# Performance work log

Hardware: AMD Instinct MI355X
Metric: run time of the kernel (lower is better)

Reference implementation:

```python
import jax, jax.numpy as jnp
import numpy as np

B, S, H, NH = 2, 2048, 4096, 32
HD = H // NH  # head_dim = 128
ROPE_BASE = 10000.0


def setup_inputs() -> dict:
    key = jax.random.key(0)
    k1, k2, k3 = jax.random.split(key, 3)
    hidden_states = jax.random.normal(k1, (B, S, H), dtype=jnp.float32)
    w_qkv = jax.random.normal(k2, (H, 3 * H), dtype=jnp.float32) * 0.02
    w_o = jax.random.normal(k3, (H, H), dtype=jnp.float32) * 0.02
    position_ids = jnp.broadcast_to(jnp.arange(S, dtype=jnp.int32), (B, S))
    return {"hidden_states": hidden_states, "w_qkv": w_qkv, "w_o": w_o,
            "position_ids": position_ids}


def _rope_neox(x, cos, sin):
    # x: [B,S,NH,HD]; cos/sin: [B,S,1,HD//2]. NeoX rotate-halves.
    half = HD // 2
    x1, x2 = x[..., :half], x[..., half:]
    return jnp.concatenate([x1 * cos - x2 * sin, x2 * cos + x1 * sin], axis=-1)


def reference(hidden_states, w_qkv, w_o, position_ids):
    # fused QKV projection (stands in for quantized WQLinear)
    qkv = hidden_states @ w_qkv                        # [B,S,3H]
    q, k, v = jnp.split(qkv, 3, axis=-1)
    q = q.reshape(B, S, NH, HD)
    k = k.reshape(B, S, NH, HD)
    v = v.reshape(B, S, NH, HD)

    # NeoX rotary embedding indexed by position_ids
    inv_freq = 1.0 / (ROPE_BASE ** (jnp.arange(0, HD, 2, dtype=jnp.float32) / HD))
    freqs = position_ids.astype(jnp.float32)[..., None] * inv_freq  # [B,S,HD/2]
    cos = jnp.cos(freqs)[:, :, None, :]
    sin = jnp.sin(freqs)[:, :, None, :]
    q = _rope_neox(q, cos, sin)
    k = _rope_neox(k, cos, sin)

    # causal SDPA (prefill path: past_key_value is None -> is_causal=True)
    scale = 1.0 / jnp.sqrt(jnp.asarray(HD, dtype=q.dtype))
    scores = jnp.einsum('bqhd,bkhd->bhqk', q, k) * scale  # [B,NH,S,S]
    causal = jnp.tril(jnp.ones((S, S), dtype=bool))
    scores = jnp.where(causal, scores, jnp.finfo(scores.dtype).min)
    probs = jax.nn.softmax(scores, axis=-1)
    attn = jnp.einsum('bhqk,bkhd->bqhd', probs, v).reshape(B, S, H)

    return attn @ w_o  # [B,S,H]
```

## Files before the change

kernel.cpp:

```cpp
#include <hip/hip_runtime.h>
#include <stdint.h>
#include <math.h>

#define B_ 2
#define S_ 2048
#define H_ 4096
#define NH_ 32
#define HD_ 128

using s16x8 = __attribute__((ext_vector_type(8))) short;
using f32x4 = __attribute__((ext_vector_type(4))) float;

__device__ __forceinline__ unsigned short f2b(float f) {
  union { float f; unsigned u; } v; v.f = f;
  unsigned r = v.u + 0x7FFFu + ((v.u >> 16) & 1u);
  return (unsigned short)(r >> 16);
}
__device__ __forceinline__ unsigned short f2b_trunc(float f) {
  union { float f; unsigned u; } v; v.f = f;
  return (unsigned short)(v.u >> 16);
}
__device__ __forceinline__ float b2f(unsigned short h) {
  union { unsigned u; float f; } v; v.u = ((unsigned)h) << 16;
  return v.f;
}

__device__ __forceinline__ void async_cp16(const void* g, void* l) {
  __builtin_amdgcn_global_load_lds(
      (__attribute__((address_space(1))) void*)(void*)g,
      (__attribute__((address_space(3))) void*)l, 16, 0, 0);
}

#define MFMA16(a, b, c) __builtin_amdgcn_mfma_f32_16x16x32_bf16((a), (b), (c), 0, 0, 0)
#define BARRIER() asm volatile("s_barrier" ::: "memory")

__global__ void cast_f32_bf16(const float* __restrict__ in,
                              unsigned short* __restrict__ out, long n) {
  long i = ((long)blockIdx.x * 256 + threadIdx.x) * 4;
  if (i >= n) return;
  const float4 v = *(const float4*)(in + i);
  ushort4 o;
  o.x = f2b(v.x); o.y = f2b(v.y); o.z = f2b(v.z); o.w = f2b(v.w);
  *(ushort4*)(out + i) = o;
}

__global__ void transpose_cast_4096(const float* __restrict__ in,
                                    unsigned short* __restrict__ out, int in_stride) {
  __shared__ unsigned tile[64][33];
  const int t = threadIdx.x;
  const int c0 = blockIdx.x * 64;
  const int r0 = blockIdx.y * 64;
  const int l16 = t & 15, q = t >> 4;
  const int c4 = l16 * 4;
#pragma unroll
  for (int ii = 0; ii < 2; ii++) {
    const int p = q + ii * 16;
    const float4 ra = *(const float4*)&in[(long)(r0 + 2 * p) * in_stride + c0 + c4];
    const float4 rb = *(const float4*)&in[(long)(r0 + 2 * p + 1) * in_stride + c0 + c4];
    tile[c4 + 0][p] = (unsigned)f2b(ra.x) | ((unsigned)f2b(rb.x) << 16);
    tile[c4 + 1][p] = (unsigned)f2b(ra.y) | ((unsigned)f2b(rb.y) << 16);
    tile[c4 + 2][p] = (unsigned)f2b(ra.z) | ((unsigned)f2b(rb.z) << 16);
    tile[c4 + 3][p] = (unsigned)f2b(ra.w) | ((unsigned)f2b(rb.w) << 16);
  }
  __syncthreads();
  const int c = t >> 2, r8 = (t & 3) * 8;
  unsigned v[8];
#pragma unroll
  for (int k = 0; k < 8; k++) v[k] = tile[c][r8 + k];
  uint4 o0 = {v[0], v[1], v[2], v[3]};
  uint4 o1 = {v[4], v[5], v[6], v[7]};
  unsigned short* dst = &out[(long)(c0 + c) * 4096 + r0 + 2 * r8];
  *(uint4*)dst = o0;
  *(uint4*)(dst + 8) = o1;
}

template <int MODE>
__global__ __launch_bounds__(512, 2) void gemm_bt(
    const unsigned short* __restrict__ A,
    const unsigned short* __restrict__ Bt,
    float* __restrict__ Cf,
    unsigned short* __restrict__ Dst,
    int M, int N, int K) {
  __shared__ __align__(16) unsigned short lds[65536];
  const int tid = threadIdx.x;
  const int lane = tid & 63;
  const int w = tid >> 6;
  const int quad = lane >> 4, l16 = lane & 15;
  const int wm = w >> 2, wn = w & 3;

  const int id = blockIdx.x;
  const int swz = (id & 7) * 32 + (id >> 3);
  const int m0 = (swz >> 4) * 256;
  const int n0 = (swz & 15) * 256;

  const int lr = tid >> 3;
  const int c8 = (tid & 7) * 8;
  const int csw = c8 ^ (((lr >> 1) & 7) << 3);
  const unsigned short* gA = A + (long)(m0 + lr) * K + csw;
  const unsigned short* gB = Bt + (long)(n0 + lr) * K + csw;
  const long K64 = (long)K * 64;
  const int ldsS = lr * 64 + c8;

  const int fsw = ((l16 >> 1) & 7) << 3;
  const int colk0 = (quad * 8) ^ fsw;
  const int colk1 = colk0 ^ 32;
  const int aoff0 = (wm * 128 + l16) * 64 + colk0;
  const int aoff1 = (wm * 128 + l16) * 64 + colk1;
  const int boff0 = 32768 + (wn * 64 + l16) * 64 + colk0;
  const int boff1 = 32768 + (wn * 64 + l16) * 64 + colk1;

  const f32x4 z4 = {0.f, 0.f, 0.f, 0.f};
  f32x4 acc[8][4];
#pragma unroll
  for (int mi = 0; mi < 8; mi++)
#pragma unroll
    for (int ni = 0; ni < 4; ni++) acc[mi][ni] = z4;

  async_cp16(gB, &lds[32768 + ldsS]);
  async_cp16(gB + K64, &lds[32768 + ldsS + 4096]);
  async_cp16(gB + 2 * K64, &lds[32768 + 8192 + ldsS]);
  async_cp16(gB + 3 * K64, &lds[32768 + 8192 + ldsS + 4096]);
  async_cp16(gA, &lds[ldsS]);
  async_cp16(gA + K64, &lds[ldsS + 4096]);
  async_cp16(gA + 2 * K64, &lds[8192 + ldsS]);
  async_cp16(gA + 3 * K64, &lds[8192 + ldsS + 4096]);
  async_cp16(gB + 64, &lds[32768 + 16384 + ldsS]);
  async_cp16(gB + 64 + K64, &lds[32768 + 16384 + ldsS + 4096]);
  async_cp16(gB + 64 + 2 * K64, &lds[32768 + 16384 + 8192 + ldsS]);
  async_cp16(gB + 64 + 3 * K64, &lds[32768 + 16384 + 8192 + ldsS + 4096]);
  asm volatile("s_waitcnt vmcnt(4)\n\ts_barrier" ::: "memory");

  const int NT = 64;
  for (int t = 0; t < NT; ++t) {
    const int buf = (t & 1) * 16384;
    const int nbuf = 16384 - buf;
    const long kA = (long)(t + 1) * 64;
    const long kB = (long)(t + 2) * 64;
    s16x8 a[4][2], b0[2][2], b1[2][2];

#pragma unroll
    for (int mi = 0; mi < 4; ++mi) {
      a[mi][0] = *(const s16x8*)&lds[buf + aoff0 + mi * 1024];
      a[mi][1] = *(const s16x8*)&lds[buf + aoff1 + mi * 1024];
    }
#pragma unroll
    for (int ni = 0; ni < 2; ++ni) {
      b0[ni][0] = *(const s16x8*)&lds[buf + boff0 + ni * 1024];
      b0[ni][1] = *(const s16x8*)&lds[buf + boff1 + ni * 1024];
    }
    if (t < NT - 1) {
      async_cp16(gA + kA, &lds[nbuf + ldsS]);
      async_cp16(gA + kA + K64, &lds[nbuf + ldsS + 4096]);
    }
    BARRIER();
    __builtin_amdgcn_s_setprio(1);
#pragma unroll
    for (int mi = 0; mi < 4; ++mi)
#pragma unroll
      for (int ni = 0; ni < 2; ++ni) {
        acc[mi][ni] = MFMA16(a[mi][0], b0[ni][0], acc[mi][ni]);
        acc[mi][ni] = MFMA16(a[mi][1], b0[ni][1], acc[mi][ni]);
      }
    __builtin_amdgcn_s_setprio(0);
    BARRIER();

#pragma unroll
    for (int ni = 0; ni < 2; ++ni) {
      b1[ni][0] = *(const s16x8*)&lds[buf + boff0 + (ni + 2) * 1024];
      b1[ni][1] = *(const s16x8*)&lds[buf + boff1 + (ni + 2) * 1024];
    }
    if (t < NT - 1) {
      async_cp16(gA + kA + 2 * K64, &lds[nbuf + 8192 + ldsS]);
      async_cp16(gA + kA + 3 * K64, &lds[nbuf + 8192 + ldsS + 4096]);
    }
    BARRIER();
    __builtin_amdgcn_s_setprio(1);
#pragma unroll
    for (int mi = 0; mi < 4; ++mi)
#pragma unroll
      for (int ni = 0; ni < 2; ++ni) {
        acc[mi][ni + 2] = MFMA16(a[mi][0], b1[ni][0], acc[mi][ni + 2]);
        acc[mi][ni + 2] = MFMA16(a[mi][1], b1[ni][1], acc[mi][ni + 2]);
      }
    __builtin_amdgcn_s_setprio(0);
    BARRIER();

#pragma unroll
    for (int mi = 0; mi < 4; ++mi) {
      a[mi][0] = *(const s16x8*)&lds[buf + aoff0 + (mi + 4) * 1024];
      a[mi][1] = *(const s16x8*)&lds[buf + aoff1 + (mi + 4) * 1024];
    }
    if (t < NT - 2) {
      async_cp16(gB + kB, &lds[32768 + buf + ldsS]);
      async_cp16(gB + kB + K64, &lds[32768 + buf + ldsS + 4096]);
    }
    BARRIER();
    __builtin_amdgcn_s_setprio(1);
#pragma unroll
    for (int mi = 0; mi < 4; ++mi)
#pragma unroll
      for (int ni = 0; ni < 2; ++ni) {
        acc[mi + 4][ni + 2] = MFMA16(a[mi][0], b1[ni][0], acc[mi + 4][ni + 2]);
        acc[mi + 4][ni + 2] = MFMA16(a[mi][1], b1[ni][1], acc[mi + 4][ni + 2]);
      }
    __builtin_amdgcn_s_setprio(0);
    BARRIER();

    if (t < NT - 2) {
      async_cp16(gB + kB + 2 * K64, &lds[32768 + buf + 8192 + ldsS]);
      async_cp16(gB + kB + 3 * K64, &lds[32768 + buf + 8192 + ldsS + 4096]);
    }
    BARRIER();
    __builtin_amdgcn_s_setprio(1);
#pragma unroll
    for (int mi = 0; mi < 4; ++mi)
#pragma unroll
      for (int ni = 0; ni < 2; ++ni) {
        acc[mi + 4][ni] = MFMA16(a[mi][0], b0[ni][0], acc[mi + 4][ni]);
        acc[mi + 4][ni] = MFMA16(a[mi][1], b0[ni][1], acc[mi + 4][ni]);
      }
    __builtin_amdgcn_s_setprio(0);
    if (t < NT - 2) {
      asm volatile("s_waitcnt vmcnt(4)\n\ts_barrier" ::: "memory");
    } else if (t == NT - 2) {
      asm volatile("s_waitcnt vmcnt(0)\n\ts_barrier" ::: "memory");
    } else {
      BARRIER();
    }
  }

#pragma unroll
  for (int mi = 0; mi < 8; ++mi)
#pragma unroll
    for (int ni = 0; ni < 4; ++ni) {
      const int row = m0 + wm * 128 + mi * 16 + quad * 4;
      const int col = n0 + wn * 64 + ni * 16 + l16;
      if (MODE == 0) {
#pragma unroll
        for (int r = 0; r < 4; ++r)
          Cf[(long)(row + r) * N + col] = acc[mi][ni][r];
      } else {
        const int h = col >> 7, d = col & 127;
#pragma unroll
        for (int r = 0; r < 4; ++r) {
          const int m = row + r;
          const int b = m >> 11, s = m & 2047;
          Dst[((long)((b * NH_ + h) * S_) + s) * HD_ + d] = f2b(acc[mi][ni][r]);
        }
      }
    }
}

__global__ void rope_kernel(unsigned short* __restrict__ Qb,
                            unsigned short* __restrict__ Kb,
                            const int* __restrict__ pos_ids) {
  const float QSCALE = 1.4426950408889634f * 0.08838834764831845f;
  const long idx = (long)blockIdx.x * 256 + threadIdx.x;
  const int i = (int)(idx & 63);
  const long row = idx >> 6;
  const int s = (int)(row & (S_ - 1));
  const long bh = row >> 11;
  const int b = (int)(bh >> 5);
  const float pos = (float)pos_ids[b * S_ + s];
  const float inv = exp2f(-(float)i * 0.20762050593046f);
  const float ang = pos * inv;
  const float sn = sinf(ang), cs = cosf(ang);
  const long base = row * HD_;
  const float q1 = b2f(Qb[base + i]), q2 = b2f(Qb[base + 64 + i]);
  Qb[base + i] = f2b((q1 * cs - q2 * sn) * QSCALE);
  Qb[base + 64 + i] = f2b((q2 * cs + q1 * sn) * QSCALE);
  const float k1 = b2f(Kb[base + i]), k2 = b2f(Kb[base + 64 + i]);
  Kb[base + i] = f2b(k1 * cs - k2 * sn);
  Kb[base + 64 + i] = f2b(k2 * cs + k1 * sn);
}

__global__ void transpose_v(const unsigned short* __restrict__ V,
                            unsigned short* __restrict__ Vt) {
  __shared__ unsigned short tile[64][66];
  const int bh = blockIdx.z;
  const int s0 = blockIdx.x * 64;
  const int d0 = blockIdx.y * 64;
  const unsigned short* src = V + (long)bh * S_ * HD_;
  unsigned short* dst = Vt + (long)bh * S_ * HD_;
  const int tx = threadIdx.x & 63, ty = threadIdx.x >> 6;
#pragma unroll
  for (int i = 0; i < 64; i += 4)
    tile[ty + i][tx] = src[(long)(s0 + ty + i) * HD_ + d0 + tx];
  __syncthreads();
#pragma unroll
  for (int i = 0; i < 64; i += 4)
    dst[(long)(d0 + ty + i) * S_ + s0 + tx] = tile[tx][ty + i];
}

__global__ __launch_bounds__(256, 2) void flash_attn(
    const unsigned short* __restrict__ Qb,
    const unsigned short* __restrict__ Kb,
    const unsigned short* __restrict__ Vt,
    unsigned short* __restrict__ Ab) {
  __shared__ __align__(16) unsigned short Ks[16 * 64 * 8];
  __shared__ __align__(16) unsigned short Vs[8 * 128 * 8];
  __shared__ __align__(16) unsigned short plds[128 * 72];
  const int tid = threadIdx.x;
  const int w = tid >> 6, lane = tid & 63;
  const int quad = lane >> 4, l16 = lane & 15;
  const int qx = blockIdx.y;
  const int bh = blockIdx.x;
  const int b = bh >> 5, h = bh & 31;

  const unsigned short* Qh = Qb + (long)bh * S_ * HD_;
  const unsigned short* Kh = Kb + (long)bh * S_ * HD_;
  const unsigned short* Vh = Vt + (long)bh * S_ * HD_;

  const unsigned short* kstage = Kh + (long)(tid & 63) * HD_ + (tid >> 6) * 8;
  const unsigned short* vstage = Vh + (long)(tid & 127) * S_ + (tid >> 7) * 8;

  const f32x4 z4 = {0.f, 0.f, 0.f, 0.f};
  s16x8 onesv;
#pragma unroll
  for (int j = 0; j < 8; j++) onesv[j] = (short)0x3F80;

  for (int half = 0; half < 2; half++) {
    const int qt = half ? qx : 15 - qx;
    const int q0 = qt * 128;
    const int wq = q0 + w * 32;

    s16x8 qf[2][4];
#pragma unroll
    for (int rb = 0; rb < 2; rb++)
#pragma unroll
      for (int ks = 0; ks < 4; ks++)
        qf[rb][ks] = *(const s16x8*)(Qh + (long)(wq + rb * 16 + l16) * HD_ + ks * 32 + quad * 8);

    f32x4 oacc[2][8];
    f32x4 lacc[2];
#pragma unroll
    for (int rb = 0; rb < 2; rb++) {
#pragma unroll
      for (int oc = 0; oc < 8; oc++) oacc[rb][oc] = z4;
      lacc[rb] = z4;
    }
    float mrow[2][4];
#pragma unroll
    for (int rb = 0; rb < 2; rb++)
#pragma unroll
      for (int r = 0; r < 4; r++) mrow[rb][r] = -3.0e38f;

    const int nkt = 2 * qt + 2;

    for (int kt = 0; kt < nkt; kt++) {
      const int kbase = kt * 64;
      __syncthreads();
#pragma unroll
      for (int j = 0; j < 4; j++)
        async_cp16(kstage + (long)kbase * HD_ + j * 32, &Ks[(j * 256 + tid) * 8]);
#pragma unroll
      for (int j = 0; j < 4; j++)
        async_cp16(vstage + kbase + j * 16, &Vs[(j * 256 + tid) * 8]);
      __syncthreads();

      const bool active = (kbase < wq + 32);
      if (active) {
        f32x4 sacc[2][4];
#pragma unroll
        for (int rb = 0; rb < 2; rb++)
#pragma unroll
          for (int ni = 0; ni < 4; ni++) sacc[rb][ni] = z4;
        __builtin_amdgcn_s_setprio(1);
#pragma unroll
        for (int ni = 0; ni < 4; ni++) {
#pragma unroll
          for (int ks = 0; ks < 4; ks++) {
            const s16x8 kf = *(const s16x8*)&Ks[((ks * 4 + quad) * 64 + ni * 16 + l16) * 8];
            sacc[0][ni] = MFMA16(qf[0][ks], kf, sacc[0][ni]);
            sacc[1][ni] = MFMA16(qf[1][ks], kf, sacc[1][ni]);
          }
        }
        __builtin_amdgcn_s_setprio(0);

        const bool band = (kbase + 64 > wq);
        float pm[2][4];
        bool small_ = true;
#pragma unroll
        for (int rb = 0; rb < 2; rb++) {
          const int rloc = w * 32 + rb * 16 + quad * 4;
          if (band) {
#pragma unroll
            for (int ni = 0; ni < 4; ni++)
#pragma unroll
              for (int r = 0; r < 4; r++)
                if (kbase + ni * 16 + l16 > q0 + rloc + r) sacc[rb][ni][r] = -3.0e38f;
          }
#pragma unroll
          for (int r = 0; r < 4; r++) {
            pm[rb][r] = fmaxf(fmaxf(sacc[rb][0][r], sacc[rb][1][r]),
                              fmaxf(sacc[rb][2][r], sacc[rb][3][r]));
            small_ = small_ && (pm[rb][r] <= mrow[rb][r] + 8.0f);
          }
        }
        const bool nores = __all(small_);

        if (!nores) {
#pragma unroll
          for (int rb = 0; rb < 2; rb++) {
            float alpha[4];
#pragma unroll
            for (int r = 0; r < 4; r++) {
              float m = pm[rb][r];
#pragma unroll
              for (int off = 1; off < 16; off <<= 1) m = fmaxf(m, __shfl_xor(m, off));
              const float mn = fmaxf(mrow[rb][r], m);
              alpha[r] = __builtin_amdgcn_exp2f(mrow[rb][r] - mn);
              mrow[rb][r] = mn;
            }
#pragma unroll
            for (int oc = 0; oc < 8; oc++)
#pragma unroll
              for (int r = 0; r < 4; r++) oacc[rb][oc][r] *= alpha[r];
#pragma unroll
            for (int r = 0; r < 4; r++) lacc[rb][r] *= alpha[r];
          }
        }

#pragma unroll
        for (int rb = 0; rb < 2; rb++) {
          const int rloc = w * 32 + rb * 16 + quad * 4;
#pragma unroll
          for (int ni = 0; ni < 4; ni++)
#pragma unroll
            for (int r = 0; r < 4; r++) {
              const float p = __builtin_amdgcn_exp2f(sacc[rb][ni][r] - mrow[rb][r]);
              plds[(rloc + r) * 72 + ni * 16 + l16] = f2b_trunc(p);
            }
        }

        s16x8 af[2][2];
#pragma unroll
        for (int rb = 0; rb < 2; rb++)
#pragma unroll
          for (int ks = 0; ks < 2; ks++)
            af[rb][ks] = *(const s16x8*)&plds[(w * 32 + rb * 16 + l16) * 72 + ks * 32 + quad * 8];
        __builtin_amdgcn_s_setprio(1);
#pragma unroll
        for (int rb = 0; rb < 2; rb++) {
          lacc[rb] = MFMA16(af[rb][0], onesv, lacc[rb]);
          lacc[rb] = MFMA16(af[rb][1], onesv, lacc[rb]);
        }
#pragma unroll
        for (int oc = 0; oc < 8; oc++) {
#pragma unroll
          for (int ks = 0; ks < 2; ks++) {
            const s16x8 vf = *(const s16x8*)&Vs[((ks * 4 + quad) * 128 + oc * 16 + l16) * 8];
            oacc[0][oc] = MFMA16(af[0][ks], vf, oacc[0][oc]);
            oacc[1][oc] = MFMA16(af[1][ks], vf, oacc[1][oc]);
          }
        }
        __builtin_amdgcn_s_setprio(0);
      }
    }

#pragma unroll
    for (int rb = 0; rb < 2; rb++) {
      float inv_l[4];
#pragma unroll
      for (int r = 0; r < 4; r++) inv_l[r] = 1.f / lacc[rb][r];
#pragma unroll
      for (int oc = 0; oc < 8; oc++)
#pragma unroll
        for (int r = 0; r < 4; r++) {
          const int s = q0 + w * 32 + rb * 16 + quad * 4 + r;
          const int d = oc * 16 + l16;
          Ab[((long)(b * S_ + s)) * H_ + h * HD_ + d] = f2b(oacc[rb][oc][r] * inv_l[r]);
        }
    }
  }
}

extern "C" void kernel_launch(void* const* d_in, const int* in_sizes, int n_in,
                              void* d_out, int out_size, void* d_ws, size_t ws_size,
                              hipStream_t stream) {
  const float* hs = (const float*)d_in[0];
  const float* w_qkv = (const float*)d_in[1];
  const float* w_o = (const float*)d_in[2];
  const int* pos = (const int*)d_in[3];
  float* out = (float*)d_out;

  const long EL = (long)4096 * 4096;
  unsigned short* Xb = (unsigned short*)d_ws;
  unsigned short* Wt = Xb + EL;
  unsigned short* Qb = Wt + EL;
  unsigned short* Kb = Qb + EL;
  unsigned short* Vb = Kb + EL;
  unsigned short* Vt = Vb + EL;
  unsigned short* Ab = Xb;

  cast_f32_bf16<<<(EL / 4 + 255) / 256, 256, 0, stream>>>(hs, Xb, EL);

  unsigned short* qkv_dst[3] = {Qb, Kb, Vb};
  for (int p = 0; p < 3; p++) {
    transpose_cast_4096<<<dim3(64, 64), 256, 0, stream>>>(w_qkv + p * 4096, Wt, 12288);
    gemm_bt<1><<<dim3(256), dim3(512), 0, stream>>>(Xb, Wt, nullptr, qkv_dst[p], 4096, 4096, 4096);
  }

  rope_kernel<<<(B_ * NH_ * S_ * 64) / 256, 256, 0, stream>>>(Qb, Kb, pos);
  transpose_v<<<dim3(32, 2, 64), 256, 0, stream>>>(Vb, Vt);
  flash_attn<<<dim3(64, 8), 256, 0, stream>>>(Qb, Kb, Vt, Ab);

  transpose_cast_4096<<<dim3(64, 64), 256, 0, stream>>>(w_o, Wt, 4096);
  gemm_bt<0><<<dim3(256), dim3(512), 0, stream>>>(Ab, Wt, out, nullptr, 4096, 4096, 4096);
}
```

Baseline: 960.1 us.

## Prefetch next K/V tile during attention compute and restage GEMM A/B loads

The flash attention kernel now double-buffers V in shared memory and issues the next tile's K and V async copies right after QK^T, so global loads overlap the softmax and PV MFMAs instead of stalling at the top of each iteration. The GEMM main loop is reorganised so the A and B tiles for step t+2 are issued in two bursts of four copies into the buffer being consumed, with the wait threshold raised to vmcnt(8). These changes are meant to hide global-to-LDS latency. The cost is more shared memory in attention and more outstanding loads and register pressure in the GEMM, which could reduce occupancy.

```diff
diff --git a/kernel.cpp b/kernel.cpp
--- a/kernel.cpp
+++ b/kernel.cpp
@@ -128,14 +128,16 @@
   async_cp16(gB + 64 + K64, &lds[32768 + 16384 + ldsS + 4096]);
   async_cp16(gB + 64 + 2 * K64, &lds[32768 + 16384 + 8192 + ldsS]);
   async_cp16(gB + 64 + 3 * K64, &lds[32768 + 16384 + 8192 + ldsS + 4096]);
-  asm volatile("s_waitcnt vmcnt(4)\n\ts_barrier" ::: "memory");
+  async_cp16(gA + 64, &lds[16384 + ldsS]);
+  async_cp16(gA + 64 + K64, &lds[16384 + ldsS + 4096]);
+  async_cp16(gA + 64 + 2 * K64, &lds[16384 + 8192 + ldsS]);
+  async_cp16(gA + 64 + 3 * K64, &lds[16384 + 8192 + ldsS + 4096]);
+  asm volatile("s_waitcnt vmcnt(8)\n\ts_barrier" ::: "memory");
 
   const int NT = 64;
   for (int t = 0; t < NT; ++t) {
     const int buf = (t & 1) * 16384;
-    const int nbuf = 16384 - buf;
-    const long kA = (long)(t + 1) * 64;
-    const long kB = (long)(t + 2) * 64;
+    const long kT2 = (long)(t + 2) * 64;
     s16x8 a[4][2], b0[2][2], b1[2][2];
 
 #pragma unroll
@@ -148,10 +150,6 @@
       b0[ni][0] = *(const s16x8*)&lds[buf + boff0 + ni * 1024];
       b0[ni][1] = *(const s16x8*)&lds[buf + boff1 + ni * 1024];
     }
-    if (t < NT - 1) {
-      async_cp16(gA + kA, &lds[nbuf + ldsS]);
-      async_cp16(gA + kA + K64, &lds[nbuf + ldsS + 4096]);
-    }
     BARRIER();
     __builtin_amdgcn_s_setprio(1);
 #pragma unroll
@@ -169,10 +167,6 @@
       b1[ni][0] = *(const s16x8*)&lds[buf + boff0 + (ni + 2) * 1024];
       b1[ni][1] = *(const s16x8*)&lds[buf + boff1 + (ni + 2) * 1024];
     }
-    if (t < NT - 1) {
-      async_cp16(gA + kA + 2 * K64, &lds[nbuf + 8192 + ldsS]);
-      async_cp16(gA + kA + 3 * K64, &lds[nbuf + 8192 + ldsS + 4096]);
-    }
     BARRIER();
     __builtin_amdgcn_s_setprio(1);
 #pragma unroll
@@ -191,8 +185,10 @@
       a[mi][1] = *(const s16x8*)&lds[buf + aoff1 + (mi + 4) * 1024];
     }
     if (t < NT - 2) {
-      async_cp16(gB + kB, &lds[32768 + buf + ldsS]);
-      async_cp16(gB + kB + K64, &lds[32768 + buf + ldsS + 4096]);
+      async_cp16(gB + kT2, &lds[32768 + buf + ldsS]);
+      async_cp16(gB + kT2 + K64, &lds[32768 + buf + ldsS + 4096]);
+      async_cp16(gB + kT2 + 2 * K64, &lds[32768 + buf + 8192 + ldsS]);
+      async_cp16(gB + kT2 + 3 * K64, &lds[32768 + buf + 8192 + ldsS + 4096]);
     }
     BARRIER();
     __builtin_amdgcn_s_setprio(1);
@@ -207,8 +203,10 @@
     BARRIER();
 
     if (t < NT - 2) {
-      async_cp16(gB + kB + 2 * K64, &lds[32768 + buf + 8192 + ldsS]);
-      async_cp16(gB + kB + 3 * K64, &lds[32768 + buf + 8192 + ldsS + 4096]);
+      async_cp16(gA + kT2, &lds[buf + ldsS]);
+      async_cp16(gA + kT2 + K64, &lds[buf + ldsS + 4096]);
+      async_cp16(gA + kT2 + 2 * K64, &lds[buf + 8192 + ldsS]);
+      async_cp16(gA + kT2 + 3 * K64, &lds[buf + 8192 + ldsS + 4096]);
     }
     BARRIER();
     __builtin_amdgcn_s_setprio(1);
@@ -221,7 +219,7 @@
       }
     __builtin_amdgcn_s_setprio(0);
     if (t < NT - 2) {
-      asm volatile("s_waitcnt vmcnt(4)\n\ts_barrier" ::: "memory");
+      asm volatile("s_waitcnt vmcnt(8)\n\ts_barrier" ::: "memory");
     } else if (t == NT - 2) {
       asm volatile("s_waitcnt vmcnt(0)\n\ts_barrier" ::: "memory");
     } else {
@@ -298,7 +296,7 @@
     const unsigned short* __restrict__ Vt,
     unsigned short* __restrict__ Ab) {
   __shared__ __align__(16) unsigned short Ks[16 * 64 * 8];
-  __shared__ __align__(16) unsigned short Vs[8 * 128 * 8];
+  __shared__ __align__(16) unsigned short Vs[2][8 * 128 * 8];
   __shared__ __align__(16) unsigned short plds[128 * 72];
   const int tid = threadIdx.x;
   const int w = tid >> 6, lane = tid & 63;
@@ -319,6 +317,15 @@
 #pragma unroll
   for (int j = 0; j < 8; j++) onesv[j] = (short)0x3F80;
 
+#pragma unroll
+  for (int j = 0; j < 4; j++)
+    async_cp16(kstage + j * 32, &Ks[(j * 256 + tid) * 8]);
+#pragma unroll
+  for (int j = 0; j < 4; j++)
+    async_cp16(vstage + j * 16, &Vs[0][(j * 256 + tid) * 8]);
+  asm volatile("s_waitcnt vmcnt(0)" ::: "memory");
+  __syncthreads();
+
   for (int half = 0; half < 2; half++) {
     const int qt = half ? qx : 15 - qx;
     const int q0 = qt * 128;
@@ -349,18 +356,11 @@
 
     for (int kt = 0; kt < nkt; kt++) {
       const int kbase = kt * 64;
-      __syncthreads();
-#pragma unroll
-      for (int j = 0; j < 4; j++)
-        async_cp16(kstage + (long)kbase * HD_ + j * 32, &Ks[(j * 256 + tid) * 8]);
-#pragma unroll
-      for (int j = 0; j < 4; j++)
-        async_cp16(vstage + kbase + j * 16, &Vs[(j * 256 + tid) * 8]);
-      __syncthreads();
-
+      const int cur = kt & 1;
       const bool active = (kbase < wq + 32);
+
+      f32x4 sacc[2][4];
       if (active) {
-        f32x4 sacc[2][4];
 #pragma unroll
         for (int rb = 0; rb < 2; rb++)
 #pragma unroll
@@ -376,7 +376,21 @@
           }
         }
         __builtin_amdgcn_s_setprio(0);
-
+      }
+      __syncthreads();
+
+      const bool more = (kt + 1 < nkt);
+      if (more || half == 0) {
+        const long nkb = more ? (long)(kbase + 64) : 0;
+#pragma unroll
+        for (int j = 0; j < 4; j++)
+          async_cp16(kstage + nkb * HD_ + j * 32, &Ks[(j * 256 + tid) * 8]);
+#pragma unroll
+        for (int j = 0; j < 4; j++)
+          async_cp16(vstage + nkb + j * 16, &Vs[1 - cur][(j * 256 + tid) * 8]);
+      }
+
+      if (active) {
         const bool band = (kbase + 64 > wq);
         float pm[2][4];
         bool small_ = true;
@@ -449,13 +463,16 @@
         for (int oc = 0; oc < 8; oc++) {
 #pragma unroll
           for (int ks = 0; ks < 2; ks++) {
-            const s16x8 vf = *(const s16x8*)&Vs[((ks * 4 + quad) * 128 + oc * 16 + l16) * 8];
+            const s16x8 vf = *(const s16x8*)&Vs[cur][((ks * 4 + quad) * 128 + oc * 16 + l16) * 8];
             oacc[0][oc] = MFMA16(af[0][ks], vf, oacc[0][oc]);
             oacc[1][oc] = MFMA16(af[1][ks], vf, oacc[1][oc]);
           }
         }
         __builtin_amdgcn_s_setprio(0);
       }
+
+      asm volatile("s_waitcnt vmcnt(0)" ::: "memory");
+      __syncthreads();
     }
 
 #pragma unroll
```

Measured after the change: 963.8 us. No clear change (+0.4%).
